# Performance work log

Measured on AMD Instinct MI355X. Metric: run time of the kernel, lower is better.

## Reference

```python
import jax, jax.numpy as jnp
import numpy as np

B, N, C, H = 4, 1024, 768, 12
D = C // H  # head_dim = 64


def setup_inputs() -> dict:
    key = jax.random.key(0)
    ks = jax.random.split(key, 16)
    def lin(k, fan_in, fan_out):
        # torch Linear init: U(-1/sqrt(fan_in), 1/sqrt(fan_in)); stored as [in, out]
        bound = 1.0 / np.sqrt(fan_in)
        kw, kb = jax.random.split(k)
        W = jax.random.uniform(kw, (fan_in, fan_out), minval=-bound, maxval=bound, dtype=jnp.float32)
        b = jax.random.uniform(kb, (fan_out,), minval=-bound, maxval=bound, dtype=jnp.float32)
        return W, b
    Wq, bq = lin(ks[0], C, C)
    Wk, bk = lin(ks[1], C, C)
    Wv, bv = lin(ks[2], C, C)
    Wo, bo = lin(ks[3], C, C)
    Wd1, bd1 = lin(ks[4], 1, 16)
    Wd2, bd2 = lin(ks[5], 16, H)
    x = jax.random.normal(ks[6], (B, N, C), dtype=jnp.float32)
    coords = jax.random.uniform(ks[7], (B, N, 2), dtype=jnp.float32)
    return {"x": x, "coords": coords,
            "Wq": Wq, "bq": bq, "Wk": Wk, "bk": bk, "Wv": Wv, "bv": bv,
            "Wo": Wo, "bo": bo, "Wd1": Wd1, "bd1": bd1, "Wd2": Wd2, "bd2": bd2}


def reference(x, coords, Wq, bq, Wk, bk, Wv, bv, Wo, bo, Wd1, bd1, Wd2, bd2):
    scale = D ** (-0.5)
    # projections -> [B, H, N, D]
    def heads(t):
        return t.reshape(B, N, H, D).transpose(0, 2, 1, 3)
    q = heads(x @ Wq + bq)
    k = heads(x @ Wk + bk)
    v = heads(x @ Wv + bv)
    # content scores [B, H, N, N]
    content = jnp.einsum('bhid,bhjd->bhij', q, k) * scale
    # pairwise distances [B, N, N, 1]
    diff = coords[:, :, None, :] - coords[:, None, :, :]
    dist = jnp.sqrt(jnp.sum(diff * diff, axis=-1, keepdims=True) + 1e-6)
    # distance MLP: 1 -> 16 -> H, then permute to [B, H, N, N]
    hbias = jax.nn.relu(dist @ Wd1 + bd1)
    spatial = (hbias @ Wd2 + bd2).transpose(0, 3, 1, 2)
    attn = jax.nn.softmax(content + spatial, axis=-1)
    out = jnp.einsum('bhij,bhjd->bhid', attn, v)
    out = out.transpose(0, 2, 1, 3).reshape(B, N, C)
    out = out @ Wo + bo
    return out, attn
```

## Files before the change

### kernel.cpp

```cpp
#include <hip/hip_runtime.h>
#include <cstddef>
#include <cstdint>

#define Bc 4
#define Nc 1024
#define Cc 768
#define Hc 12
#define Dc 64
#define BHc 48
#define QKV_ELEMS ((size_t)Bc * Nc * Cc)

typedef __attribute__((ext_vector_type(4))) unsigned int u32x4;
typedef __attribute__((ext_vector_type(2))) unsigned int u32x2;
typedef __attribute__((ext_vector_type(8))) short s16x8;
typedef __attribute__((ext_vector_type(8))) _Float16 h16x8;
typedef __attribute__((ext_vector_type(4))) float fx4;
typedef __attribute__((ext_vector_type(2))) float fx2;

union Frag { u32x4 u; s16x8 s; h16x8 f16; unsigned short h[8]; };
union H4 { u32x2 d; _Float16 h[4]; };

__device__ inline unsigned short f2bf(float x) {
    union { float f; uint32_t u; } c; c.f = x;
    return (unsigned short)((c.u + 0x7FFFu + ((c.u >> 16) & 1u)) >> 16);
}
__device__ inline float bf2f(unsigned short b) {
    union { uint32_t u; float f; } c; c.u = ((uint32_t)b) << 16;
    return c.f;
}
__device__ inline void split8(const float* v, u32x4& hi, u32x4& lo) {
    Frag fh, fl;
    #pragma unroll
    for (int e = 0; e < 8; ++e) {
        const unsigned short hb = f2bf(v[e]);
        fh.h[e] = hb;
        fl.h[e] = f2bf(v[e] - bf2f(hb));
    }
    hi = fh.u; lo = fl.u;
}
__device__ inline void split8h(const float* v, u32x4& hi, u32x4& lo) {
    Frag fh, fl;
    #pragma unroll
    for (int e = 0; e < 8; ++e) {
        const _Float16 hb = (_Float16)v[e];
        fh.f16[e] = hb;
        fl.f16[e] = (_Float16)(v[e] - (float)hb);
    }
    hi = fh.u; lo = fl.u;
}

__global__ __launch_bounds__(256) void prep_w_kernel(
    const float* __restrict__ Wq, const float* __restrict__ Wk,
    const float* __restrict__ Wv, const float* __restrict__ Wo,
    unsigned short* __restrict__ Thi, unsigned short* __restrict__ Tlo)
{
    __shared__ float scr[64 * 65];
    const int mat = blockIdx.z;
    const float* W = (mat == 0) ? Wq : (mat == 1) ? Wk : (mat == 2) ? Wv : Wo;
    const int k0 = blockIdx.y * 64, n0 = blockIdx.x * 64;
    const int tid = threadIdx.x;

    #pragma unroll
    for (int it = 0; it < 4; ++it) {
        const int lin = tid + it * 256;
        const int r = lin >> 4, c4 = (lin & 15) << 2;
        const fx4 v = *(const fx4*)&W[(size_t)(k0 + r) * 768 + n0 + c4];
        scr[r * 65 + c4 + 0] = v[0]; scr[r * 65 + c4 + 1] = v[1];
        scr[r * 65 + c4 + 2] = v[2]; scr[r * 65 + c4 + 3] = v[3];
    }
    __syncthreads();
    unsigned short* th = Thi + (size_t)mat * 768 * 768;
    unsigned short* tl = Tlo + (size_t)mat * 768 * 768;
    #pragma unroll
    for (int it = 0; it < 16; ++it) {
        const int lin = tid + it * 256;
        const int n = lin >> 6, kq = lin & 63;
        const float val = scr[kq * 65 + n];
        const size_t o = (size_t)(n0 + n) * 768 + k0 + kq;
        const unsigned short hb = f2bf(val);
        th[o] = hb;
        tl[o] = f2bf(val - bf2f(hb));
    }
}

__global__ __launch_bounds__(256) void prep_tables_kernel(
    const float* __restrict__ Wd1, const float* __restrict__ bd1,
    const float* __restrict__ Wd2, const float* __restrict__ bd2,
    float* __restrict__ abPack, unsigned char* __restrict__ lut)
{
    __shared__ float w1s[16], b1s[16], kn[16];
    __shared__ int rank[16];
    const int tid = threadIdx.x;
    if (tid < 16) {
        const float w1 = Wd1[tid], b1 = bd1[tid];
        w1s[tid] = w1; b1s[tid] = b1;
        kn[tid] = (w1 != 0.0f) ? (-b1 / w1) : INFINITY;
    }
    __syncthreads();
    if (tid < 16) {
        int rk = 0;
        for (int u = 0; u < 16; ++u) {
            const float ku = kn[u], km = kn[tid];
            if (ku < km || (ku == km && u < tid)) ++rk;
        }
        rank[tid] = rk;
    }
    __syncthreads();
    if (tid < 17 * 12) {
        const int s = tid / 12, h = tid % 12;
        float a = 0.0f, be = bd2[h];
        for (int u = 0; u < 16; ++u) {
            const float w1 = w1s[u], b1 = b1s[u];
            bool act;
            if (w1 > 0.0f)      act = (rank[u] < s);
            else if (w1 < 0.0f) act = (rank[u] >= s);
            else                act = (b1 > 0.0f);
            if (act) {
                const float w2 = Wd2[u * 12 + h];
                a  += w2 * w1;
                be += w2 * b1;
            }
        }
        abPack[tid * 2 + 0] = a;
        abPack[tid * 2 + 1] = be;
    }
    for (int b = tid; b < 2048; b += 256) {
        const float rep = (b + 0.5f) * (1.41422f / 2048.0f);
        int cnt = 0;
        for (int t = 0; t < 16; ++t) cnt += (rep > kn[t]) ? 1 : 0;
        lut[b] = (unsigned char)cnt;
    }
}

__global__ __launch_bounds__(256) void split_x_kernel(
    const float* __restrict__ x, unsigned short* __restrict__ xhi,
    unsigned short* __restrict__ xlo)
{
    const size_t t = (size_t)blockIdx.x * 256 + threadIdx.x;
    float vv[8];
    const fx4 a = *(const fx4*)&x[t * 8];
    const fx4 b = *(const fx4*)&x[t * 8 + 4];
    vv[0]=a[0]; vv[1]=a[1]; vv[2]=a[2]; vv[3]=a[3];
    vv[4]=b[0]; vv[5]=b[1]; vv[6]=b[2]; vv[7]=b[3];
    u32x4 hi, lo; split8(vv, hi, lo);
    *(u32x4*)&xhi[t * 8] = hi;
    *(u32x4*)&xlo[t * 8] = lo;
}

struct SmemG { u32x4 ah[512]; u32x4 al[512]; u32x4 bh[512]; u32x4 bl[512]; };
struct SmemT { float scr[64 * 68]; };
union SmemU { SmemG g; SmemT t; };

template<int OMODE>
__global__ __launch_bounds__(256) void gemm_mfma_kernel(
    const unsigned short* __restrict__ Ahi, const unsigned short* __restrict__ Alo,
    const unsigned short* __restrict__ Bhi, const unsigned short* __restrict__ Blo,
    const float* __restrict__ bias,
    float* __restrict__ outF,
    unsigned short* __restrict__ Ohi, unsigned short* __restrict__ Olo)
{
    __shared__ SmemU sm;
    const int tid = threadIdx.x;
    const int w = tid >> 6, L = tid & 63;
    const int Lr = L & 15, Lg = L >> 4;
    const int m0 = blockIdx.y * 64, n0 = blockIdx.x * 64;

    fx4 acc[2][2] = {};

    for (int kk = 0; kk < 768; kk += 64) {
        #pragma unroll
        for (int it = 0; it < 2; ++it) {
            const int slot = tid + it * 256;
            const int s = slot >> 6, l = slot & 63;
            const int row = m0 + ((s >> 1) << 4) + (l & 15);
            const int kb = kk + ((s & 1) << 5) + ((l >> 4) << 3);
            sm.g.ah[slot] = *(const u32x4*)&Ahi[(size_t)row * 768 + kb];
            sm.g.al[slot] = *(const u32x4*)&Alo[(size_t)row * 768 + kb];
            const int col = n0 + ((s >> 1) << 4) + (l & 15);
            sm.g.bh[slot] = *(const u32x4*)&Bhi[(size_t)col * 768 + kb];
            sm.g.bl[slot] = *(const u32x4*)&Blo[(size_t)col * 768 + kb];
        }
        __syncthreads();
        #pragma unroll
        for (int kc = 0; kc < 2; ++kc) {
            Frag ah[2], al[2], bh[2], bl[2];
            #pragma unroll
            for (int mm = 0; mm < 2; ++mm) {
                const int rg = (w >> 1) * 2 + mm;
                ah[mm].u = sm.g.ah[(rg * 2 + kc) * 64 + L];
                al[mm].u = sm.g.al[(rg * 2 + kc) * 64 + L];
            }
            #pragma unroll
            for (int nn = 0; nn < 2; ++nn) {
                const int cg = (w & 1) * 2 + nn;
                bh[nn].u = sm.g.bh[(cg * 2 + kc) * 64 + L];
                bl[nn].u = sm.g.bl[(cg * 2 + kc) * 64 + L];
            }
            #pragma unroll
            for (int mm = 0; mm < 2; ++mm)
                #pragma unroll
                for (int nn = 0; nn < 2; ++nn) {
                    acc[mm][nn] = __builtin_amdgcn_mfma_f32_16x16x32_bf16(ah[mm].s, bh[nn].s, acc[mm][nn], 0, 0, 0);
                    acc[mm][nn] = __builtin_amdgcn_mfma_f32_16x16x32_bf16(ah[mm].s, bl[nn].s, acc[mm][nn], 0, 0, 0);
                    acc[mm][nn] = __builtin_amdgcn_mfma_f32_16x16x32_bf16(al[mm].s, bh[nn].s, acc[mm][nn], 0, 0, 0);
                }
        }
        __syncthreads();
    }

    #pragma unroll
    for (int mm = 0; mm < 2; ++mm) {
        const int rl = (w >> 1) * 32 + mm * 16 + Lg * 4;
        #pragma unroll
        for (int nn = 0; nn < 2; ++nn) {
            const int cl = (w & 1) * 32 + nn * 16 + Lr;
            const float bs = bias[n0 + cl];
            #pragma unroll
            for (int r = 0; r < 4; ++r)
                sm.t.scr[(rl + r) * 68 + cl] = acc[mm][nn][r] + bs;
        }
    }
    __syncthreads();

    if (OMODE == 0) {
        const int h = n0 >> 6;
        #pragma unroll
        for (int it = 0; it < 2; ++it) {
            const int t = tid + it * 256;
            const int r = t >> 3, d0 = (t & 7) << 3;
            float vv[8];
            #pragma unroll
            for (int e = 0; e < 8; ++e) vv[e] = sm.t.scr[r * 68 + d0 + e];
            u32x4 hi, lo; split8(vv, hi, lo);
            const int rg = m0 + r, b = rg >> 10, nloc = rg & 1023;
            const size_t o = (((size_t)(b * Hc + h) * Nc + nloc) << 6) + d0;
            *(u32x4*)&Ohi[o] = hi;
            *(u32x4*)&Olo[o] = lo;
        }
    } else if (OMODE == 1) {
        const int b = m0 >> 10, h = n0 >> 6, nbase = m0 & 1023;
        #pragma unroll
        for (int it = 0; it < 2; ++it) {
            const int t = tid + it * 256;
            const int dd = t >> 3, j0 = (t & 7) << 3;
            float vv[8];
            #pragma unroll
            for (int e = 0; e < 8; ++e) vv[e] = sm.t.scr[(j0 + e) * 68 + dd];
            u32x4 hi, lo; split8h(vv, hi, lo);
            const size_t o = (size_t)((b * Hc + h) * Dc + dd) * Nc + nbase + j0;
            *(u32x4*)&Ohi[o] = hi;
            *(u32x4*)&Olo[o] = lo;
        }
    } else {
        #pragma unroll
        for (int it = 0; it < 4; ++it) {
            const int lin = tid + it * 256;
            const int r = lin >> 4, c4 = (lin & 15) << 2;
            const fx4 v = *(const fx4*)&sm.t.scr[r * 68 + c4];
            *(fx4*)&outF[(size_t)(m0 + r) * 768 + n0 + c4] = v;
        }
    }
}

union FlashSmem {
    struct { u32x4 vh[512]; u32x4 vl[512]; char escr[4 * 2048]; } p;
    float scr[64 * 68];
};

__global__ __launch_bounds__(256) void attn_flash_kernel(
    const unsigned short* __restrict__ qhi, const unsigned short* __restrict__ qlo,
    const unsigned short* __restrict__ khi, const unsigned short* __restrict__ klo,
    const unsigned short* __restrict__ vThi, const unsigned short* __restrict__ vTlo,
    const float* __restrict__ coords,
    const float* __restrict__ abPack, const unsigned char* __restrict__ lutg,
    unsigned short* __restrict__ e_ws, float* __restrict__ mT,
    float* __restrict__ mlfin,
    unsigned short* __restrict__ Hphi, unsigned short* __restrict__ Hplo)
{
    __shared__ FlashSmem sm;
    __shared__ fx2 cjs[1024];
    __shared__ unsigned char luts[2048];
    __shared__ fx2 abt[17];

    const int tid = threadIdx.x;
    const int w = tid >> 6, L = tid & 63;
    const int Lr = L & 15, Lg = L >> 4;
    const int bh = blockIdx.y, b = bh / Hc, h = bh % Hc;
    const int i0 = blockIdx.x * 64;
    const int i = i0 + w * 16 + Lr;
    const int Lg4 = Lg * 4;

    if (tid < 17) abt[tid] = ((const fx2*)abPack)[tid * Hc + h];
    for (int t = tid; t < 512; t += 256)
        ((uint32_t*)luts)[t] = ((const uint32_t*)lutg)[t];
    for (int t = tid; t < 1024; t += 256)
        cjs[t] = *(const fx2*)&coords[((size_t)b * Nc + t) * 2];

    Frag qh[2], ql[2];
    #pragma unroll
    for (int kc = 0; kc < 2; ++kc) {
        const size_t o = ((size_t)bh * Nc + i) * 64 + kc * 32 + Lg * 8;
        qh[kc].u = *(const u32x4*)&qhi[o];
        ql[kc].u = *(const u32x4*)&qlo[o];
    }
    const fx2 ci = *(const fx2*)&coords[((size_t)b * Nc + i) * 2];
    __syncthreads();

    char* eb = sm.p.escr + w * 2048;
    fx4 oacc[4] = {};
    float m_r = -INFINITY, l_r = 0.f;

    for (int jt = 0; jt < 16; ++jt) {
        const int jbase = jt * 64;

        u32x4 vsh[2], vsl[2];
        #pragma unroll
        for (int it = 0; it < 2; ++it) {
            const int s = tid + it * 256;
            const int l = s & 63;
            const int dd = ((s >> 7) << 4) + (l & 15);
            const int jo = jbase + ((s >> 6) & 1) * 32 + ((l >> 4) << 3);
            const size_t off = ((size_t)bh * Dc + dd) * Nc + jo;
            vsh[it] = *(const u32x4*)&vThi[off];
            vsl[it] = *(const u32x4*)&vTlo[off];
        }

        fx4 acc[4] = {};
        #pragma unroll
        for (int kc = 0; kc < 2; ++kc) {
            Frag kh[4], kl[4];
            #pragma unroll
            for (int cg = 0; cg < 4; ++cg) {
                const size_t o = ((size_t)bh * Nc + jbase + cg * 16 + Lr) * 64 + kc * 32 + Lg * 8;
                kh[cg].u = *(const u32x4*)&khi[o];
                kl[cg].u = *(const u32x4*)&klo[o];
            }
            #pragma unroll
            for (int cg = 0; cg < 4; ++cg) {
                acc[cg] = __builtin_amdgcn_mfma_f32_16x16x32_bf16(kh[cg].s, qh[kc].s, acc[cg], 0, 0, 0);
                acc[cg] = __builtin_amdgcn_mfma_f32_16x16x32_bf16(kl[cg].s, qh[kc].s, acc[cg], 0, 0, 0);
                acc[cg] = __builtin_amdgcn_mfma_f32_16x16x32_bf16(kh[cg].s, ql[kc].s, acc[cg], 0, 0, 0);
            }
        }

        float sv[16];
        #pragma unroll
        for (int cg = 0; cg < 4; ++cg) {
            #pragma unroll
            for (int r = 0; r < 4; ++r) {
                const fx2 cj = cjs[jbase + cg * 16 + Lg4 + r];
                const float dx = ci[0] - cj[0], dy = ci[1] - cj[1];
                const float dist = sqrtf(fmaf(dx, dx, fmaf(dy, dy, 1e-6f)));
                int bin = (int)(dist * (2048.0f / 1.41422f));
                bin = (bin > 2047) ? 2047 : bin;
                const fx2 ab = abt[luts[bin]];
                sv[cg * 4 + r] = fmaf(acc[cg][r], 0.125f, fmaf(ab[0], dist, ab[1]));
            }
        }

        float tm = sv[0];
        #pragma unroll
        for (int e = 1; e < 16; ++e) tm = fmaxf(tm, sv[e]);
        tm = fmaxf(tm, __shfl_xor(tm, 16));
        tm = fmaxf(tm, __shfl_xor(tm, 32));

        float ts = 0.f;
        #pragma unroll
        for (int e = 0; e < 16; ++e) { sv[e] = __expf(sv[e] - tm); ts += sv[e]; }
        ts += __shfl_xor(ts, 16);
        ts += __shfl_xor(ts, 32);

        if (Lg == 0) mT[((size_t)bh * Nc + i) * 16 + jt] = tm;

        __syncthreads();
        #pragma unroll
        for (int it = 0; it < 2; ++it) {
            const int s = tid + it * 256;
            sm.p.vh[s] = vsh[it];
            sm.p.vl[s] = vsl[it];
        }
        #pragma unroll
        for (int cg = 0; cg < 4; ++cg) {
            H4 pk;
            #pragma unroll
            for (int r = 0; r < 4; ++r) pk.h[r] = (_Float16)sv[cg * 4 + r];
            const int g = cg * 4 + Lg;
            const int waddr = ((g >> 3) << 10) + (((((g & 7) >> 1) << 4) + Lr) << 4) + ((g & 1) << 3);
            *(u32x2*)(eb + waddr) = pk.d;
        }
        __syncthreads();

        const float mnew = fmaxf(m_r, tm);
        const float facc = __expf(m_r - mnew);
        const float ftile = __expf(tm - mnew);
        l_r = l_r * facc + ts * ftile;
        m_r = mnew;
        #pragma unroll
        for (int r = 0; r < 4; ++r) {
            const float fr = __shfl(facc, Lg4 + r);
            #pragma unroll
            for (int dg = 0; dg < 4; ++dg) oacc[dg][r] *= fr;
        }
        const _Float16 fh = (_Float16)ftile;

        const size_t ebase_g = (size_t)((bh * 16 + jt) * 2) * 32768 + (size_t)i * 32 + Lg * 8;
        #pragma unroll
        for (int kc = 0; kc < 2; ++kc) {
            Frag eA;
            eA.u = *(const u32x4*)(eb + kc * 1024 + (L << 4));
            *(u32x4*)&e_ws[ebase_g + (size_t)kc * 32768] = eA.u;
            Frag pa;
            pa.f16 = eA.f16 * fh;
            #pragma unroll
            for (int dg = 0; dg < 4; ++dg) {
                Frag vh_, vl_;
                vh_.u = sm.p.vh[(dg * 2 + kc) * 64 + L];
                vl_.u = sm.p.vl[(dg * 2 + kc) * 64 + L];
                oacc[dg] = __builtin_amdgcn_mfma_f32_16x16x32_f16(pa.f16, vh_.f16, oacc[dg], 0, 0, 0);
                oacc[dg] = __builtin_amdgcn_mfma_f32_16x16x32_f16(pa.f16, vl_.f16, oacc[dg], 0, 0, 0);
            }
        }
    }

    const float il = 1.0f / l_r;
    if (Lg == 0) *(fx2*)&mlfin[2 * ((size_t)bh * Nc + i)] = fx2{m_r, il};

    float il4[4];
    #pragma unroll
    for (int r = 0; r < 4; ++r) il4[r] = __shfl(il, Lg4 + r);

    __syncthreads();
    #pragma unroll
    for (int dg = 0; dg < 4; ++dg)
        #pragma unroll
        for (int r = 0; r < 4; ++r)
            sm.scr[(w * 16 + Lg4 + r) * 68 + dg * 16 + Lr] = oacc[dg][r] * il4[r];
    __syncthreads();

    #pragma unroll
    for (int it = 0; it < 2; ++it) {
        const int lin = tid + it * 256;
        const int row = lin >> 3, d0 = (lin & 7) << 3;
        float vv[8];
        #pragma unroll
        for (int e = 0; e < 8; ++e) vv[e] = sm.scr[row * 68 + d0 + e];
        u32x4 hi, lo; split8(vv, hi, lo);
        const size_t o = ((size_t)b * Nc + i0 + row) * Cc + h * Dc + d0;
        *(u32x4*)&Hphi[o] = hi;
        *(u32x4*)&Hplo[o] = lo;
    }
}

__global__ __launch_bounds__(256) void norm_kernel(
    const unsigned short* __restrict__ e_ws,
    const float* __restrict__ mT, const float* __restrict__ mlfin,
    float* __restrict__ attn)
{
    const size_t t = (size_t)blockIdx.x * 256 + threadIdx.x;
    const int blk = (int)(t >> 10);
    const int i = (int)(t & 1023);
    const int bh = blk >> 5;
    const int jt = (blk >> 1) & 15;
    const int kc = blk & 1;
    const size_t row = (size_t)bh * Nc + i;

    const fx2 mf = *(const fx2*)&mlfin[2 * row];
    const float mt = mT[row * 16 + jt];
    const float f = __expf(mt - mf[0]) * mf[1];

    const unsigned short* ep = &e_ws[(size_t)blk * 32768 + (size_t)i * 32];
    float* ap = &attn[row * Nc + jt * 64 + kc * 32];
    #pragma unroll
    for (int c = 0; c < 4; ++c) {
        Frag ev;
        ev.u = *(const u32x4*)&ep[c * 8];
        fx4 o0, o1;
        o0[0] = (float)ev.f16[0] * f; o0[1] = (float)ev.f16[1] * f;
        o0[2] = (float)ev.f16[2] * f; o0[3] = (float)ev.f16[3] * f;
        o1[0] = (float)ev.f16[4] * f; o1[1] = (float)ev.f16[5] * f;
        o1[2] = (float)ev.f16[6] * f; o1[3] = (float)ev.f16[7] * f;
        *(fx4*)&ap[c * 8] = o0;
        *(fx4*)&ap[c * 8 + 4] = o1;
    }
}

extern "C" void kernel_launch(void* const* d_in, const int* in_sizes, int n_in,
                              void* d_out, int out_size, void* d_ws, size_t ws_size,
                              hipStream_t stream)
{
    (void)in_sizes; (void)n_in; (void)out_size; (void)ws_size;

    const float* x      = (const float*)d_in[0];
    const float* coords = (const float*)d_in[1];
    const float* Wq = (const float*)d_in[2];  const float* bq = (const float*)d_in[3];
    const float* Wk = (const float*)d_in[4];  const float* bk = (const float*)d_in[5];
    const float* Wv = (const float*)d_in[6];  const float* bv = (const float*)d_in[7];
    const float* Wo = (const float*)d_in[8];  const float* bo = (const float*)d_in[9];
    const float* Wd1 = (const float*)d_in[10]; const float* bd1 = (const float*)d_in[11];
    const float* Wd2 = (const float*)d_in[12]; const float* bd2 = (const float*)d_in[13];

    float* out_main = (float*)d_out;
    float* attn     = out_main + QKV_ELEMS;

    uint8_t* wsb = (uint8_t*)d_ws;
    const size_t SZ_BF = (size_t)BHc * Nc * Dc * 2;
    const size_t SZ_W4 = (size_t)4 * 768 * 768 * 2;
    unsigned short* qhi  = (unsigned short*)(wsb + 0 * SZ_BF);
    unsigned short* qlo  = (unsigned short*)(wsb + 1 * SZ_BF);
    unsigned short* khi  = (unsigned short*)(wsb + 2 * SZ_BF);
    unsigned short* klo  = (unsigned short*)(wsb + 3 * SZ_BF);
    unsigned short* vThi = (unsigned short*)(wsb + 4 * SZ_BF);
    unsigned short* vTlo = (unsigned short*)(wsb + 5 * SZ_BF);
    unsigned short* xhi  = (unsigned short*)(wsb + 6 * SZ_BF);
    unsigned short* xlo  = (unsigned short*)(wsb + 7 * SZ_BF);
    unsigned short* Thi  = (unsigned short*)(wsb + 8 * SZ_BF);
    unsigned short* Tlo  = (unsigned short*)(wsb + 8 * SZ_BF + SZ_W4);
    uint8_t* base8 = wsb + 8 * SZ_BF + 2 * SZ_W4;
    float* abPack = (float*)base8;
    unsigned char* lut = (unsigned char*)(base8 + 4096);
    float* mT    = (float*)(base8 + 8192);
    float* mlfin = mT + (size_t)BHc * Nc * 16;
    unsigned short* e_ws = (unsigned short*)(mlfin + (size_t)BHc * Nc * 2);

    prep_w_kernel<<<dim3(12, 12, 4), 256, 0, stream>>>(Wq, Wk, Wv, Wo, Thi, Tlo);
    prep_tables_kernel<<<1, 256, 0, stream>>>(Wd1, bd1, Wd2, bd2, abPack, lut);
    split_x_kernel<<<dim3(1536), 256, 0, stream>>>(x, xhi, xlo);

    dim3 gGemm(12, 64);
    gemm_mfma_kernel<0><<<gGemm, 256, 0, stream>>>(
        xhi, xlo, Thi + (size_t)0 * 768 * 768, Tlo + (size_t)0 * 768 * 768,
        bq, nullptr, qhi, qlo);
    gemm_mfma_kernel<0><<<gGemm, 256, 0, stream>>>(
        xhi, xlo, Thi + (size_t)1 * 768 * 768, Tlo + (size_t)1 * 768 * 768,
        bk, nullptr, khi, klo);
    gemm_mfma_kernel<1><<<gGemm, 256, 0, stream>>>(
        xhi, xlo, Thi + (size_t)2 * 768 * 768, Tlo + (size_t)2 * 768 * 768,
        bv, nullptr, vThi, vTlo);

    attn_flash_kernel<<<dim3(16, 48), 256, 0, stream>>>(
        qhi, qlo, khi, klo, vThi, vTlo, coords, abPack, lut,
        e_ws, mT, mlfin, xhi, xlo);

    norm_kernel<<<dim3(6144), 256, 0, stream>>>(e_ws, mT, mlfin, attn);

    gemm_mfma_kernel<2><<<gGemm, 256, 0, stream>>>(
        xhi, xlo, Thi + (size_t)3 * 768 * 768, Tlo + (size_t)3 * 768 * 768,
        bo, out_main, nullptr, nullptr);
}
```

Baseline: 417.5 us.

## Fuse attention normalization into flash kernel and double-buffer V tiles

Removes the separate norm kernel. Per-tile maxima and the final m/1/l values now stay in shared memory, and each block rescales its own e_ws rows into attn at the end of the flash kernel. V tiles are double-buffered in LDS with a prologue load, so one of the two barriers per tile goes away. The exp-tile values are written straight to global from registers instead of being staged through LDS, and the PV product switches to 16x16x16 f16 MFMAs fed directly from registers. Coordinates are read from global instead of LDS. The price is more global traffic from the CU doing the normalization, plus re-reading e_ws within the same kernel.

```diff
diff --git a/kernel.cpp b/kernel.cpp
--- a/kernel.cpp
+++ b/kernel.cpp
@@ -14,11 +14,12 @@
 typedef __attribute__((ext_vector_type(2))) unsigned int u32x2;
 typedef __attribute__((ext_vector_type(8))) short s16x8;
 typedef __attribute__((ext_vector_type(8))) _Float16 h16x8;
+typedef __attribute__((ext_vector_type(4))) _Float16 h16x4;
 typedef __attribute__((ext_vector_type(4))) float fx4;
 typedef __attribute__((ext_vector_type(2))) float fx2;
 
 union Frag { u32x4 u; s16x8 s; h16x8 f16; unsigned short h[8]; };
-union H4 { u32x2 d; _Float16 h[4]; };
+union H4b { u32x2 d; h16x4 h4; };
 
 __device__ inline unsigned short f2bf(float x) {
     union { float f; uint32_t u; } c; c.f = x;
@@ -262,10 +263,8 @@
     }
 }
 
-union FlashSmem {
-    struct { u32x4 vh[512]; u32x4 vl[512]; char escr[4 * 2048]; } p;
-    float scr[64 * 68];
-};
+struct VBuf { u32x4 vh[512]; u32x4 vl[512]; };
+union FlashSmem { VBuf vbuf[2]; float scr[64 * 68]; };
 
 __global__ __launch_bounds__(256) void attn_flash_kernel(
     const unsigned short* __restrict__ qhi, const unsigned short* __restrict__ qlo,
@@ -273,12 +272,13 @@
     const unsigned short* __restrict__ vThi, const unsigned short* __restrict__ vTlo,
     const float* __restrict__ coords,
     const float* __restrict__ abPack, const unsigned char* __restrict__ lutg,
-    unsigned short* __restrict__ e_ws, float* __restrict__ mT,
-    float* __restrict__ mlfin,
+    unsigned short* __restrict__ e_ws,
+    float* __restrict__ attn,
     unsigned short* __restrict__ Hphi, unsigned short* __restrict__ Hplo)
 {
     __shared__ FlashSmem sm;
-    __shared__ fx2 cjs[1024];
+    __shared__ float mTs[64][17];
+    __shared__ float ms[64], ils[64];
     __shared__ unsigned char luts[2048];
     __shared__ fx2 abt[17];
 
@@ -287,14 +287,13 @@
     const int Lr = L & 15, Lg = L >> 4;
     const int bh = blockIdx.y, b = bh / Hc, h = bh % Hc;
     const int i0 = blockIdx.x * 64;
-    const int i = i0 + w * 16 + Lr;
+    const int iloc = w * 16 + Lr;
+    const int i = i0 + iloc;
     const int Lg4 = Lg * 4;
 
     if (tid < 17) abt[tid] = ((const fx2*)abPack)[tid * Hc + h];
     for (int t = tid; t < 512; t += 256)
         ((uint32_t*)luts)[t] = ((const uint32_t*)lutg)[t];
-    for (int t = tid; t < 1024; t += 256)
-        cjs[t] = *(const fx2*)&coords[((size_t)b * Nc + t) * 2];
 
     Frag qh[2], ql[2];
     #pragma unroll
@@ -304,25 +303,39 @@
         ql[kc].u = *(const u32x4*)&qlo[o];
     }
     const fx2 ci = *(const fx2*)&coords[((size_t)b * Nc + i) * 2];
-    __syncthreads();
-
-    char* eb = sm.p.escr + w * 2048;
+    const fx2* cjall = (const fx2*)coords + (size_t)b * Nc;
+
+    #pragma unroll
+    for (int it = 0; it < 2; ++it) {
+        const int s = tid + it * 256;
+        const int l = s & 63;
+        const int dd = ((s >> 7) << 4) + (l & 15);
+        const int jo = ((s >> 6) & 1) * 32 + ((l >> 4) << 3);
+        const size_t off = ((size_t)bh * Dc + dd) * Nc + jo;
+        sm.vbuf[0].vh[s] = *(const u32x4*)&vThi[off];
+        sm.vbuf[0].vl[s] = *(const u32x4*)&vTlo[off];
+    }
+    __syncthreads();
+
     fx4 oacc[4] = {};
     float m_r = -INFINITY, l_r = 0.f;
 
     for (int jt = 0; jt < 16; ++jt) {
         const int jbase = jt * 64;
+        const int cur = jt & 1;
 
         u32x4 vsh[2], vsl[2];
-        #pragma unroll
-        for (int it = 0; it < 2; ++it) {
-            const int s = tid + it * 256;
-            const int l = s & 63;
-            const int dd = ((s >> 7) << 4) + (l & 15);
-            const int jo = jbase + ((s >> 6) & 1) * 32 + ((l >> 4) << 3);
-            const size_t off = ((size_t)bh * Dc + dd) * Nc + jo;
-            vsh[it] = *(const u32x4*)&vThi[off];
-            vsl[it] = *(const u32x4*)&vTlo[off];
+        if (jt < 15) {
+            #pragma unroll
+            for (int it = 0; it < 2; ++it) {
+                const int s = tid + it * 256;
+                const int l = s & 63;
+                const int dd = ((s >> 7) << 4) + (l & 15);
+                const int jo = jbase + 64 + ((s >> 6) & 1) * 32 + ((l >> 4) << 3);
+                const size_t off = ((size_t)bh * Dc + dd) * Nc + jo;
+                vsh[it] = *(const u32x4*)&vThi[off];
+                vsl[it] = *(const u32x4*)&vTlo[off];
+            }
         }
 
         fx4 acc[4] = {};
@@ -348,7 +361,7 @@
         for (int cg = 0; cg < 4; ++cg) {
             #pragma unroll
             for (int r = 0; r < 4; ++r) {
-                const fx2 cj = cjs[jbase + cg * 16 + Lg4 + r];
+                const fx2 cj = cjall[jbase + cg * 16 + Lg4 + r];
                 const float dx = ci[0] - cj[0], dy = ci[1] - cj[1];
                 const float dist = sqrtf(fmaf(dx, dx, fmaf(dy, dy, 1e-6f)));
                 int bin = (int)(dist * (2048.0f / 1.41422f));
@@ -370,25 +383,16 @@
         ts += __shfl_xor(ts, 16);
         ts += __shfl_xor(ts, 32);
 
-        if (Lg == 0) mT[((size_t)bh * Nc + i) * 16 + jt] = tm;
-
-        __syncthreads();
-        #pragma unroll
-        for (int it = 0; it < 2; ++it) {
-            const int s = tid + it * 256;
-            sm.p.vh[s] = vsh[it];
-            sm.p.vl[s] = vsl[it];
-        }
+        if (Lg == 0) mTs[iloc][jt] = tm;
+
+        const size_t ebase = ((size_t)(bh * 16 + jt) * 2) * 32768 + (size_t)i * 32;
         #pragma unroll
         for (int cg = 0; cg < 4; ++cg) {
-            H4 pk;
-            #pragma unroll
-            for (int r = 0; r < 4; ++r) pk.h[r] = (_Float16)sv[cg * 4 + r];
-            const int g = cg * 4 + Lg;
-            const int waddr = ((g >> 3) << 10) + (((((g & 7) >> 1) << 4) + Lr) << 4) + ((g & 1) << 3);
-            *(u32x2*)(eb + waddr) = pk.d;
-        }
-        __syncthreads();
+            H4b pk;
+            #pragma unroll
+            for (int r = 0; r < 4; ++r) pk.h4[r] = (_Float16)sv[cg * 4 + r];
+            *(u32x2*)&e_ws[ebase + (size_t)(cg >> 1) * 32768 + (cg & 1) * 16 + Lg4] = pk.d;
+        }
 
         const float mnew = fmaxf(m_r, tm);
         const float facc = __expf(m_r - mnew);
@@ -401,35 +405,47 @@
             #pragma unroll
             for (int dg = 0; dg < 4; ++dg) oacc[dg][r] *= fr;
         }
-        const _Float16 fh = (_Float16)ftile;
-
-        const size_t ebase_g = (size_t)((bh * 16 + jt) * 2) * 32768 + (size_t)i * 32 + Lg * 8;
-        #pragma unroll
-        for (int kc = 0; kc < 2; ++kc) {
-            Frag eA;
-            eA.u = *(const u32x4*)(eb + kc * 1024 + (L << 4));
-            *(u32x4*)&e_ws[ebase_g + (size_t)kc * 32768] = eA.u;
-            Frag pa;
-            pa.f16 = eA.f16 * fh;
+
+        __syncthreads();
+        if (jt < 15) {
+            #pragma unroll
+            for (int it = 0; it < 2; ++it) {
+                const int s = tid + it * 256;
+                sm.vbuf[cur ^ 1].vh[s] = vsh[it];
+                sm.vbuf[cur ^ 1].vl[s] = vsl[it];
+            }
+        }
+
+        const char* vhB = (const char*)sm.vbuf[cur].vh;
+        const char* vlB = (const char*)sm.vbuf[cur].vl;
+        #pragma unroll
+        for (int cg = 0; cg < 4; ++cg) {
+            H4b a4;
+            #pragma unroll
+            for (int r = 0; r < 4; ++r) a4.h4[r] = (_Float16)(sv[cg * 4 + r] * ftile);
+            const int sub = (cg & 1) * 2 + (Lg >> 1);
+            const int kcq = cg >> 1;
+            const int low = (Lg & 1) * 8;
             #pragma unroll
             for (int dg = 0; dg < 4; ++dg) {
-                Frag vh_, vl_;
-                vh_.u = sm.p.vh[(dg * 2 + kc) * 64 + L];
-                vl_.u = sm.p.vl[(dg * 2 + kc) * 64 + L];
-                oacc[dg] = __builtin_amdgcn_mfma_f32_16x16x32_f16(pa.f16, vh_.f16, oacc[dg], 0, 0, 0);
-                oacc[dg] = __builtin_amdgcn_mfma_f32_16x16x32_f16(pa.f16, vl_.f16, oacc[dg], 0, 0, 0);
+                const int byteoff = ((dg * 2 + kcq) * 64 + sub * 16 + Lr) * 16 + low;
+                H4b bh4, bl4;
+                bh4.d = *(const u32x2*)(vhB + byteoff);
+                bl4.d = *(const u32x2*)(vlB + byteoff);
+                oacc[dg] = __builtin_amdgcn_mfma_f32_16x16x16f16(a4.h4, bh4.h4, oacc[dg], 0, 0, 0);
+                oacc[dg] = __builtin_amdgcn_mfma_f32_16x16x16f16(a4.h4, bl4.h4, oacc[dg], 0, 0, 0);
             }
         }
     }
 
     const float il = 1.0f / l_r;
-    if (Lg == 0) *(fx2*)&mlfin[2 * ((size_t)bh * Nc + i)] = fx2{m_r, il};
-
+    if (Lg == 0) { ms[iloc] = m_r; ils[iloc] = il; }
     float il4[4];
     #pragma unroll
     for (int r = 0; r < 4; ++r) il4[r] = __shfl(il, Lg4 + r);
 
     __syncthreads();
+
     #pragma unroll
     for (int dg = 0; dg < 4; ++dg)
         #pragma unroll
@@ -449,38 +465,28 @@
         *(u32x4*)&Hphi[o] = hi;
         *(u32x4*)&Hplo[o] = lo;
     }
-}
-
-__global__ __launch_bounds__(256) void norm_kernel(
-    const unsigned short* __restrict__ e_ws,
-    const float* __restrict__ mT, const float* __restrict__ mlfin,
-    float* __restrict__ attn)
-{
-    const size_t t = (size_t)blockIdx.x * 256 + threadIdx.x;
-    const int blk = (int)(t >> 10);
-    const int i = (int)(t & 1023);
-    const int bh = blk >> 5;
-    const int jt = (blk >> 1) & 15;
-    const int kc = blk & 1;
-    const size_t row = (size_t)bh * Nc + i;
-
-    const fx2 mf = *(const fx2*)&mlfin[2 * row];
-    const float mt = mT[row * 16 + jt];
-    const float f = __expf(mt - mf[0]) * mf[1];
-
-    const unsigned short* ep = &e_ws[(size_t)blk * 32768 + (size_t)i * 32];
-    float* ap = &attn[row * Nc + jt * 64 + kc * 32];
-    #pragma unroll
-    for (int c = 0; c < 4; ++c) {
-        Frag ev;
-        ev.u = *(const u32x4*)&ep[c * 8];
-        fx4 o0, o1;
-        o0[0] = (float)ev.f16[0] * f; o0[1] = (float)ev.f16[1] * f;
-        o0[2] = (float)ev.f16[2] * f; o0[3] = (float)ev.f16[3] * f;
-        o1[0] = (float)ev.f16[4] * f; o1[1] = (float)ev.f16[5] * f;
-        o1[2] = (float)ev.f16[6] * f; o1[3] = (float)ev.f16[7] * f;
-        *(fx4*)&ap[c * 8] = o0;
-        *(fx4*)&ap[c * 8 + 4] = o1;
+
+    const int irow = tid >> 2;
+    const int jj = (tid & 3) << 3;
+    const float mrow = ms[irow], ilr = ils[irow];
+    const size_t gi = (size_t)(i0 + irow);
+    float* arow = attn + ((size_t)bh * Nc + gi) * Nc;
+    const unsigned short* ebase2 = e_ws + (size_t)(bh * 16) * 2 * 32768 + gi * 32 + jj;
+    for (int jt2 = 0; jt2 < 16; ++jt2) {
+        const float f = __expf(mTs[irow][jt2] - mrow) * ilr;
+        #pragma unroll
+        for (int kc = 0; kc < 2; ++kc) {
+            Frag ev;
+            ev.u = *(const u32x4*)(ebase2 + ((size_t)jt2 * 2 + kc) * 32768);
+            fx4 o0, o1;
+            o0[0] = (float)ev.f16[0] * f; o0[1] = (float)ev.f16[1] * f;
+            o0[2] = (float)ev.f16[2] * f; o0[3] = (float)ev.f16[3] * f;
+            o1[0] = (float)ev.f16[4] * f; o1[1] = (float)ev.f16[5] * f;
+            o1[2] = (float)ev.f16[6] * f; o1[3] = (float)ev.f16[7] * f;
+            float* ap = &arow[jt2 * 64 + kc * 32 + jj];
+            *(fx4*)ap = o0;
+            *(fx4*)(ap + 4) = o1;
+        }
     }
 }
 
@@ -518,9 +524,7 @@
     uint8_t* base8 = wsb + 8 * SZ_BF + 2 * SZ_W4;
     float* abPack = (float*)base8;
     unsigned char* lut = (unsigned char*)(base8 + 4096);
-    float* mT    = (float*)(base8 + 8192);
-    float* mlfin = mT + (size_t)BHc * Nc * 16;
-    unsigned short* e_ws = (unsigned short*)(mlfin + (size_t)BHc * Nc * 2);
+    unsigned short* e_ws = (unsigned short*)(base8 + 8192);
 
     prep_w_kernel<<<dim3(12, 12, 4), 256, 0, stream>>>(Wq, Wk, Wv, Wo, Thi, Tlo);
     prep_tables_kernel<<<1, 256, 0, stream>>>(Wd1, bd1, Wd2, bd2, abPack, lut);
@@ -539,9 +543,7 @@
 
     attn_flash_kernel<<<dim3(16, 48), 256, 0, stream>>>(
         qhi, qlo, khi, klo, vThi, vTlo, coords, abPack, lut,
-        e_ws, mT, mlfin, xhi, xlo);
-
-    norm_kernel<<<dim3(6144), 256, 0, stream>>>(e_ws, mT, mlfin, attn);
+        e_ws, attn, xhi, xlo);
 
     gemm_mfma_kernel<2><<<gGemm, 256, 0, stream>>>(
         xhi, xlo, Thi + (size_t)3 * 768 * 768, Tlo + (size_t)3 * 768 * 768,
```

Result: faster. 393.3 us (-5.8%).
